# Kernel optimization log

Hardware: AMD Instinct MI355X
Metric: run time of the kernel (lower is better)

Reference implementation:

```python
import jax, jax.numpy as jnp
import numpy as np

D_MODEL = 1024
N_HEAD = 16
B, T = 4, 1024
MAX_REL = 32  # max_relative_positions


def setup_inputs() -> dict:
    key = jax.random.key(0)
    ks = jax.random.split(key, 12)
    s = 0.02
    inp = {
        "x": jax.random.normal(ks[0], (B, T, D_MODEL), jnp.float32),
        "mask": jnp.tril(jnp.ones((T, T), dtype=bool)),  # causal mask, 1 = keep
        "Wq": jax.random.normal(ks[1], (D_MODEL, D_MODEL), jnp.float32) * s,
        "bq": jax.random.normal(ks[2], (D_MODEL,), jnp.float32) * s,
        "Wk": jax.random.normal(ks[3], (D_MODEL, D_MODEL), jnp.float32) * s,
        "bk": jax.random.normal(ks[4], (D_MODEL,), jnp.float32) * s,
        "Wv": jax.random.normal(ks[5], (D_MODEL, D_MODEL), jnp.float32) * s,
        "bv": jax.random.normal(ks[6], (D_MODEL,), jnp.float32) * s,
        "Wo": jax.random.normal(ks[7], (D_MODEL, D_MODEL), jnp.float32) * s,
        "bo": jax.random.normal(ks[8], (D_MODEL,), jnp.float32) * s,
        "rel_bias": jax.random.normal(ks[9], (2 * MAX_REL - 1, N_HEAD), jnp.float32) * s,
        "n_head": N_HEAD,
    }
    return inp


def reference(x, mask, Wq, bq, Wk, bk, Wv, bv, Wo, bo, rel_bias, n_head):
    Bx, Tx, C = x.shape
    Dh = C // n_head
    scale = Dh ** (-0.5)
    # projections: torch Linear is x @ W.T + b
    Q = (x @ Wq.T + bq).reshape(Bx, Tx, n_head, Dh)
    K = (x @ Wk.T + bk).reshape(Bx, Tx, n_head, Dh)
    V = (x @ Wv.T + bv).reshape(Bx, Tx, n_head, Dh)
    # scores: [B, H, T, T]
    scores = jnp.einsum("bqhd,bkhd->bhqk", Q, K) * scale
    # T5-style clipped relative-position bias
    pos = jnp.arange(Tx)
    rel = pos[None, :] - pos[:, None]                     # k_pos - q_pos, [T, T]
    buckets = jnp.clip(rel, -(MAX_REL - 1), MAX_REL - 1) + (MAX_REL - 1)
    bias = rel_bias[buckets]                              # [T, T, H]
    scores = scores + jnp.transpose(bias, (2, 0, 1))[None]
    # original applies masked_fill(-inf) then masked_fill(0): net effect = 0
    scores = jnp.where(mask, scores, 0.0)
    w = jax.nn.relu(scores) + 1e-6
    w = jnp.where(mask, w, 0.0)
    w = w / (jnp.sum(w, axis=-1, keepdims=True) + 1e-6)
    out = jnp.einsum("bhqk,bkhd->bqhd", w, V).reshape(Bx, Tx, C)
    return out @ Wo.T + bo
```

## Files before the change

### kernel.cpp

```cpp
#include <hip/hip_runtime.h>


typedef __attribute__((ext_vector_type(8))) __bf16 bf16x8;
typedef __attribute__((ext_vector_type(4))) __bf16 bf16x4;
typedef __attribute__((ext_vector_type(4))) float f32x4;
typedef unsigned short u16;

__device__ __forceinline__ u16 f2bf(float f) {
  unsigned u = __float_as_uint(f);
  u += 0x7FFFu + ((u >> 16) & 1u);
  return (u16)(u >> 16);
}
__device__ __forceinline__ float bf2f(u16 b) {
  return __uint_as_float(((unsigned)b) << 16);
}
__device__ __forceinline__ void gl_lds16(const void* g, void* l) {
  __builtin_amdgcn_global_load_lds((__attribute__((address_space(1))) void*)g,
                                   (__attribute__((address_space(3))) void*)l,
                                   16, 0, 0);
}

__global__ __launch_bounds__(256) void cast_all_kernel(
    const float* __restrict__ x,  const float* __restrict__ wq,
    const float* __restrict__ wk, const float* __restrict__ wv,
    const float* __restrict__ wo,
    u16* __restrict__ xb, u16* __restrict__ wqb, u16* __restrict__ wkb,
    u16* __restrict__ wvb, u16* __restrict__ wob) {
  long i4 = (long)blockIdx.x * 256 + threadIdx.x;
  const float* src; u16* dst; long rel;
  if (i4 < 1048576) { src = x; dst = xb; rel = i4; }
  else {
    long j = i4 - 1048576;
    int w = (int)(j >> 18);
    rel = j & 262143;
    src = (w == 0) ? wq : (w == 1) ? wk : (w == 2) ? wv : wo;
    dst = (w == 0) ? wqb : (w == 1) ? wkb : (w == 2) ? wvb : wob;
  }
  float4 v = ((const float4*)src)[rel];
  ushort4 o;
  o.x = f2bf(v.x); o.y = f2bf(v.y); o.z = f2bf(v.z); o.w = f2bf(v.w);
  ((ushort4*)dst)[rel] = o;
}

template <bool STORE_BF16>
__device__ __forceinline__ void gemm_body(
    const u16* __restrict__ A, const u16* __restrict__ B,
    const float* __restrict__ bias, bool rowbias,
    void* __restrict__ Cout, int ldc, int m0, int n0) {
  constexpr int K = 1024;
  constexpr int NT = K / 64;
  __shared__ __align__(16) u16 As[2][128 * 64];
  __shared__ __align__(16) u16 Bs[2][128 * 64];

  const int t = threadIdx.x;
  const int lane = t & 63;
  const int wv = t >> 6;
  const int quad = lane >> 4;
  const int l15 = lane & 15;
  const int wr = wv >> 1, wc = wv & 1;
  const int sw0 = (quad ^ (l15 & 7)) * 8;
  const int sw1 = ((4 + quad) ^ (l15 & 7)) * 8;

  const f32x4 vzero = {0.f, 0.f, 0.f, 0.f};
  f32x4 acc[4][4];
#pragma unroll
  for (int i = 0; i < 4; ++i)
#pragma unroll
    for (int j = 0; j < 4; ++j) acc[i][j] = vzero;

  auto stage = [&](int kt, int bufi) {
#pragma unroll
    for (int p = 0; p < 4; ++p) {
      int idx = t + p * 256;
      int row = idx >> 3, seg = idx & 7;
      int sseg = seg ^ (row & 7);
      gl_lds16(&A[(long)(m0 + row) * K + kt * 64 + sseg * 8], &As[bufi][idx * 8]);
      gl_lds16(&B[(long)(n0 + row) * K + kt * 64 + sseg * 8], &Bs[bufi][idx * 8]);
    }
  };

  stage(0, 0);
  for (int kt = 0; kt < NT; ++kt) {
    const int bufi = kt & 1;
    if (kt + 1 < NT) {
      stage(kt + 1, bufi ^ 1);
      asm volatile("s_waitcnt vmcnt(8)" ::: "memory");
    } else {
      asm volatile("s_waitcnt vmcnt(0)" ::: "memory");
    }
    asm volatile("s_barrier" ::: "memory");
#pragma unroll
    for (int ks = 0; ks < 64; ks += 32) {
      const int sw = ks ? sw1 : sw0;
      bf16x8 af[4], bfg[4];
#pragma unroll
      for (int i = 0; i < 4; ++i)
        af[i] = *(const bf16x8*)&As[bufi][(wr * 64 + i * 16 + l15) * 64 + sw];
#pragma unroll
      for (int j = 0; j < 4; ++j)
        bfg[j] = *(const bf16x8*)&Bs[bufi][(wc * 64 + j * 16 + l15) * 64 + sw];
#pragma unroll
      for (int i = 0; i < 4; ++i)
#pragma unroll
        for (int j = 0; j < 4; ++j)
          acc[i][j] = __builtin_amdgcn_mfma_f32_16x16x32_bf16(af[i], bfg[j], acc[i][j], 0, 0, 0);
    }
    asm volatile("s_barrier" ::: "memory");
  }

  float cb[4];
  if (!rowbias) {
#pragma unroll
    for (int j = 0; j < 4; ++j) cb[j] = bias[n0 + wc * 64 + j * 16 + l15];
  }

#pragma unroll
  for (int i = 0; i < 4; ++i) {
#pragma unroll
    for (int r = 0; r < 4; ++r) {
      int row = m0 + wr * 64 + i * 16 + quad * 4 + r;
      long base = (long)row * ldc + n0 + wc * 64;
      float rb_ = rowbias ? bias[row] : 0.f;
#pragma unroll
      for (int j = 0; j < 4; ++j) {
        float v = acc[i][j][r] + (rowbias ? rb_ : cb[j]);
        if (STORE_BF16) ((u16*)Cout)[base + j * 16 + l15] = f2bf(v);
        else            ((float*)Cout)[base + j * 16 + l15] = v;
      }
    }
  }
}

__global__ __launch_bounds__(256) void gemm_qkv(
    const u16* __restrict__ xb, const u16* __restrict__ wqb,
    const u16* __restrict__ wkb, const u16* __restrict__ wvb,
    const float* __restrict__ bq, const float* __restrict__ bk,
    const float* __restrict__ bv,
    u16* __restrict__ Qb, u16* __restrict__ Kb, u16* __restrict__ Vtg) {
  const int bx = blockIdx.x;
  const u16 *AT, *BT;
  const float* bias;
  u16* C;
  int m0, n0, ldc;
  bool rowbias;
  if (bx < 512) {
    int g = bx >> 5;
    int sel = g >> 3;
    n0 = (g & 7) * 128; m0 = (bx & 31) * 128;
    AT = xb; BT = sel ? wkb : wqb; bias = sel ? bk : bq;
    C = sel ? Kb : Qb; ldc = 1024; rowbias = false;
  } else {
    int rem = bx - 512;
    n0 = (rem >> 3) * 128; m0 = (rem & 7) * 128;
    AT = wvb; BT = xb; bias = bv;
    C = Vtg; ldc = 4096; rowbias = true;
  }
  gemm_body<true>(AT, BT, bias, rowbias, C, ldc, m0, n0);
}

__global__ __launch_bounds__(256) void gemm_out(
    const u16* __restrict__ A, const u16* __restrict__ B,
    const float* __restrict__ bias, float* __restrict__ C) {
  gemm_body<false>(A, B, bias, false, C, 1024, blockIdx.x * 128, blockIdx.y * 128);
}

__global__ __launch_bounds__(512) void attn_strip(
    const u16* __restrict__ Qb,
    const u16* __restrict__ Kb,
    const u16* __restrict__ Vtg,
    const float* __restrict__ rel_bias,
    u16* __restrict__ att) {
  constexpr int WS = 68;
  __shared__ __align__(16) u16 Kt[64 * 64];
  __shared__ __align__(16) u16 Vt[64 * 64];
  __shared__ __align__(16) u16 Ws[8][16 * WS];
  __shared__ float biasl[64];

  const int bx = blockIdx.x;
  const int strip = 7 - (bx >> 6);
  const int bh = bx & 63;
  const int b = bh >> 4, h = bh & 15;
  const int q0 = strip * 128;
  const int cend = 2 * strip + 1;

  const int t = threadIdx.x;
  const int lane = t & 63;
  const int wv = t >> 6;
  const int quad = lane >> 4;
  const int l15 = lane & 15;

  if (t < 63) biasl[t] = rel_bias[t * 16 + h];
  const float b0c = rel_bias[h];

  const long qrow = (long)(b * 1024 + q0 + wv * 16 + l15) * 1024 + h * 64;
  bf16x8 qf0 = *(const bf16x8*)&Qb[qrow + quad * 8];
  bf16x8 qf1 = *(const bf16x8*)&Qb[qrow + 32 + quad * 8];

  const f32x4 vzero = {0.f, 0.f, 0.f, 0.f};
  f32x4 acc_o[4];
#pragma unroll
  for (int j = 0; j < 4; ++j) acc_o[j] = vzero;
  float denom = 0.f;
  const float scale = 0.125f;
  const int ql = q0 + wv * 16 + l15;
  const int sw0 = (quad ^ (l15 & 7)) * 8;
  const int sw1 = ((4 + quad) ^ (l15 & 7)) * 8;

  for (int c = 0; c <= cend; ++c) {
    const int k0 = c * 64;
    if (c) __syncthreads();
    {
      int row = t >> 3, seg = t & 7;
      int sw = row * 64 + ((seg ^ (row & 7)) * 8);
      uint4 kv = *(const uint4*)&Kb[(long)(b * 1024 + k0 + row) * 1024 + h * 64 + seg * 8];
      uint4 vvl = *(const uint4*)&Vtg[(long)(h * 64 + row) * 4096 + b * 1024 + k0 + seg * 8];
      *(uint4*)&Kt[sw] = kv;
      *(uint4*)&Vt[sw] = vvl;
    }
    __syncthreads();

    const bool fast = (c <= 2 * strip - 2);
#pragma unroll
    for (int g = 0; g < 4; ++g) {
      const u16* kr = &Kt[(g * 16 + l15) * 64];
      bf16x8 kf0 = *(const bf16x8*)&kr[sw0];
      bf16x8 kf1 = *(const bf16x8*)&kr[sw1];
      f32x4 sT = vzero;
      sT = __builtin_amdgcn_mfma_f32_16x16x32_bf16(kf0, qf0, sT, 0, 0, 0);
      sT = __builtin_amdgcn_mfma_f32_16x16x32_bf16(kf1, qf1, sT, 0, 0, 0);
      const int kgb = k0 + g * 16 + quad * 4;
      ushort4 wpk;
      if (fast) {
#pragma unroll
        for (int r = 0; r < 4; ++r) {
          float w = fmaxf(sT[r] * scale + b0c, 0.f) + 1e-6f;
          u16 wb = f2bf(w);
          denom += bf2f(wb);
          ((u16*)&wpk)[r] = wb;
        }
      } else {
#pragma unroll
        for (int r = 0; r < 4; ++r) {
          int kg = kgb + r;
          int dd = kg - ql;
          dd = dd < -31 ? -31 : (dd > 31 ? 31 : dd);
          float sv = sT[r] * scale + biasl[dd + 31];
          float w = (kg <= ql) ? (fmaxf(sv, 0.f) + 1e-6f) : 0.f;
          u16 wb = f2bf(w);
          denom += bf2f(wb);
          ((u16*)&wpk)[r] = wb;
        }
      }
      *(ushort4*)&Ws[wv][l15 * WS + g * 16 + quad * 4] = wpk;
    }
    asm volatile("s_waitcnt lgkmcnt(0)" ::: "memory");
#pragma unroll
    for (int ks = 0; ks < 64; ks += 32) {
      union { bf16x8 v8; bf16x4 v4[2]; } au;
      int wbase = l15 * WS + ks + quad * 8;
      au.v4[0] = *(const bf16x4*)&Ws[wv][wbase];
      au.v4[1] = *(const bf16x4*)&Ws[wv][wbase + 4];
      const int sv = ks ? sw1 : sw0;
#pragma unroll
      for (int j = 0; j < 4; ++j) {
        bf16x8 bvv = *(const bf16x8*)&Vt[(j * 16 + l15) * 64 + sv];
        acc_o[j] = __builtin_amdgcn_mfma_f32_16x16x32_bf16(au.v8, bvv, acc_o[j], 0, 0, 0);
      }
    }
  }

  denom += __shfl_xor(denom, 16);
  denom += __shfl_xor(denom, 32);

  float invm = 1.f / (denom + 1e-6f);
  float inv[4];
#pragma unroll
  for (int r = 0; r < 4; ++r) inv[r] = __shfl(invm, quad * 4 + r);
#pragma unroll
  for (int j = 0; j < 4; ++j)
#pragma unroll
    for (int r = 0; r < 4; ++r) {
      int q = q0 + wv * 16 + quad * 4 + r;
      att[(long)(b * 1024 + q) * 1024 + h * 64 + j * 16 + l15] = f2bf(acc_o[j][r] * inv[r]);
    }
}

extern "C" void kernel_launch(void* const* d_in, const int* in_sizes, int n_in,
                              void* d_out, int out_size, void* d_ws, size_t ws_size,
                              hipStream_t stream) {
  const float* x  = (const float*)d_in[0];
  const float* Wq = (const float*)d_in[2];
  const float* bq = (const float*)d_in[3];
  const float* Wk = (const float*)d_in[4];
  const float* bk = (const float*)d_in[5];
  const float* Wv = (const float*)d_in[6];
  const float* bv = (const float*)d_in[7];
  const float* Wo = (const float*)d_in[8];
  const float* bo = (const float*)d_in[9];
  const float* rb = (const float*)d_in[10];

  char* ws = (char*)d_ws;
  u16* xb  = (u16*)(ws);
  u16* wqb = (u16*)(ws + (8l  << 20));
  u16* wkb = (u16*)(ws + (10l << 20));
  u16* wvb = (u16*)(ws + (12l << 20));
  u16* wob = (u16*)(ws + (14l << 20));
  u16* Qb  = (u16*)(ws + (16l << 20));
  u16* Kb  = (u16*)d_out;
  u16* Vtg = (u16*)((char*)d_out + (8l << 20));

  cast_all_kernel<<<8192, 256, 0, stream>>>(x, Wq, Wk, Wv, Wo, xb, wqb, wkb, wvb, wob);
  gemm_qkv<<<768, 256, 0, stream>>>(xb, wqb, wkb, wvb, bq, bk, bv, Qb, Kb, Vtg);
  attn_strip<<<512, 512, 0, stream>>>(Qb, Kb, Vtg, rb, Qb);
  gemm_out<<<dim3(32, 8), 256, 0, stream>>>(Qb, wob, bo, (float*)d_out);
}
```

Measured before the change: 191.2 us.

## Use 256x256-tile 8-wave pipelined GEMM body for QKV projection

Replaces the 128x128 QKV GEMM with a 256x256-tile, 512-thread kernel. It uses double-buffered LDS split into two k-halves, async global-to-LDS loads interleaved with MFMA phases, setprio hints, and XOR-swizzled LDS layout. Blocks are remapped so consecutive block IDs spread across XCDs. The goal is more reuse per LDS load and better overlap of loads with compute. The cost is only 192 blocks on a 256-CU part, which may leave CUs idle, plus higher register and LDS pressure.

```diff
diff --git a/kernel.cpp b/kernel.cpp
--- a/kernel.cpp
+++ b/kernel.cpp
@@ -131,31 +131,177 @@
   }
 }
 
-__global__ __launch_bounds__(256) void gemm_qkv(
+template <bool STORE_BF16>
+__device__ __forceinline__ void gemm256_body(
+    const u16* __restrict__ A, const u16* __restrict__ B,
+    const float* __restrict__ bias, bool rowbias,
+    void* __restrict__ Cout, int ldc, int m0, int n0) {
+  constexpr int K = 1024;
+  constexpr int NT = K / 64;
+  __shared__ __align__(16) u16 As[2][2][256 * 32];
+  __shared__ __align__(16) u16 Bs[2][2][256 * 32];
+
+  const int t = threadIdx.x;
+  const int lane = t & 63;
+  const int wv = t >> 6;
+  const int wr = wv >> 2;
+  const int wc = wv & 3;
+  const int quad = lane >> 4;
+  const int l15 = lane & 15;
+
+  const int rA = wr * 128 + l15;
+  const int rB = wc * 64 + l15;
+  const int baseA = rA * 32 + ((quad ^ ((rA >> 1) & 3)) * 8);
+  const int baseB = rB * 32 + ((quad ^ ((rB >> 1) & 3)) * 8);
+
+  const int srow = t >> 2;
+  const int sg = (t & 3) ^ ((t >> 3) & 3);
+  const long sA = (long)(m0 + srow) * K + sg * 8;
+  const long sB = (long)(n0 + srow) * K + sg * 8;
+
+  auto stA = [&](int T_, int kh, int bf_) {
+    const u16* s = A + sA + T_ * 64 + kh * 32;
+    u16* d = &As[bf_][kh][t * 8];
+    gl_lds16(s, d);
+    gl_lds16(s + (long)128 * K, d + 4096);
+  };
+  auto stB = [&](int T_, int kh, int bf_) {
+    const u16* s = B + sB + T_ * 64 + kh * 32;
+    u16* d = &Bs[bf_][kh][t * 8];
+    gl_lds16(s, d);
+    gl_lds16(s + (long)128 * K, d + 4096);
+  };
+
+  const f32x4 vzero = {0.f, 0.f, 0.f, 0.f};
+  f32x4 acc[8][4];
+#pragma unroll
+  for (int i = 0; i < 8; ++i)
+#pragma unroll
+    for (int j = 0; j < 4; ++j) acc[i][j] = vzero;
+
+  stA(0, 0, 0); stB(0, 0, 0);
+  stA(0, 1, 0); stB(0, 1, 0);
+  stA(1, 0, 1); stB(1, 0, 1);
+  asm volatile("s_waitcnt vmcnt(4)" ::: "memory");
+  asm volatile("s_barrier" ::: "memory");
+
+  for (int T = 0; T < NT; ++T) {
+    const int c = T & 1;
+    const u16* Ac = &As[c][0][0];
+    const u16* Bc = &Bs[c][0][0];
+    bf16x8 af[4], bfr[4];
+
+#pragma unroll
+    for (int j = 0; j < 4; ++j) bfr[j] = *(const bf16x8*)&Bc[baseB + j * 512];
+#pragma unroll
+    for (int i = 0; i < 4; ++i) af[i] = *(const bf16x8*)&Ac[baseA + i * 512];
+    if (T + 1 < NT) stA(T + 1, 1, c ^ 1);
+    asm volatile("s_barrier" ::: "memory");
+    __builtin_amdgcn_s_setprio(1);
+#pragma unroll
+    for (int i = 0; i < 4; ++i)
+#pragma unroll
+      for (int j = 0; j < 4; ++j)
+        acc[i][j] = __builtin_amdgcn_mfma_f32_16x16x32_bf16(af[i], bfr[j], acc[i][j], 0, 0, 0);
+    __builtin_amdgcn_s_setprio(0);
+    asm volatile("s_barrier" ::: "memory");
+
+#pragma unroll
+    for (int i = 0; i < 4; ++i) af[i] = *(const bf16x8*)&Ac[baseA + 2048 + i * 512];
+    if (T + 1 < NT) stB(T + 1, 1, c ^ 1);
+    asm volatile("s_barrier" ::: "memory");
+    __builtin_amdgcn_s_setprio(1);
+#pragma unroll
+    for (int i = 0; i < 4; ++i)
+#pragma unroll
+      for (int j = 0; j < 4; ++j)
+        acc[4 + i][j] = __builtin_amdgcn_mfma_f32_16x16x32_bf16(af[i], bfr[j], acc[4 + i][j], 0, 0, 0);
+    __builtin_amdgcn_s_setprio(0);
+    asm volatile("s_barrier" ::: "memory");
+
+    if (T == NT - 1) {
+      asm volatile("s_waitcnt vmcnt(0)" ::: "memory");
+      asm volatile("s_barrier" ::: "memory");
+    }
+#pragma unroll
+    for (int j = 0; j < 4; ++j) bfr[j] = *(const bf16x8*)&Bc[8192 + baseB + j * 512];
+#pragma unroll
+    for (int i = 0; i < 4; ++i) af[i] = *(const bf16x8*)&Ac[8192 + baseA + i * 512];
+    if (T + 2 < NT) stA(T + 2, 0, c);
+    asm volatile("s_barrier" ::: "memory");
+    __builtin_amdgcn_s_setprio(1);
+#pragma unroll
+    for (int i = 0; i < 4; ++i)
+#pragma unroll
+      for (int j = 0; j < 4; ++j)
+        acc[i][j] = __builtin_amdgcn_mfma_f32_16x16x32_bf16(af[i], bfr[j], acc[i][j], 0, 0, 0);
+    __builtin_amdgcn_s_setprio(0);
+    asm volatile("s_barrier" ::: "memory");
+
+#pragma unroll
+    for (int i = 0; i < 4; ++i) af[i] = *(const bf16x8*)&Ac[8192 + baseA + 2048 + i * 512];
+    if (T + 2 < NT) stB(T + 2, 0, c);
+    asm volatile("s_barrier" ::: "memory");
+    __builtin_amdgcn_s_setprio(1);
+#pragma unroll
+    for (int i = 0; i < 4; ++i)
+#pragma unroll
+      for (int j = 0; j < 4; ++j)
+        acc[4 + i][j] = __builtin_amdgcn_mfma_f32_16x16x32_bf16(af[i], bfr[j], acc[4 + i][j], 0, 0, 0);
+    __builtin_amdgcn_s_setprio(0);
+    asm volatile("s_waitcnt vmcnt(4)" ::: "memory");
+    asm volatile("s_barrier" ::: "memory");
+  }
+
+  float cb[4];
+  if (!rowbias) {
+#pragma unroll
+    for (int j = 0; j < 4; ++j) cb[j] = bias[n0 + wc * 64 + j * 16 + l15];
+  }
+
+#pragma unroll
+  for (int mf = 0; mf < 8; ++mf) {
+#pragma unroll
+    for (int r = 0; r < 4; ++r) {
+      int row = m0 + wr * 128 + mf * 16 + quad * 4 + r;
+      long base = (long)row * ldc + n0 + wc * 64;
+      float rb_ = rowbias ? bias[row] : 0.f;
+#pragma unroll
+      for (int j = 0; j < 4; ++j) {
+        float v = acc[mf][j][r] + (rowbias ? rb_ : cb[j]);
+        if (STORE_BF16) ((u16*)Cout)[base + j * 16 + l15] = f2bf(v);
+        else            ((float*)Cout)[base + j * 16 + l15] = v;
+      }
+    }
+  }
+}
+
+__global__ __launch_bounds__(512, 2) void gemm_qkv(
     const u16* __restrict__ xb, const u16* __restrict__ wqb,
     const u16* __restrict__ wkb, const u16* __restrict__ wvb,
     const float* __restrict__ bq, const float* __restrict__ bk,
     const float* __restrict__ bv,
     u16* __restrict__ Qb, u16* __restrict__ Kb, u16* __restrict__ Vtg) {
   const int bx = blockIdx.x;
+  const int L = (bx & 7) * 24 + (bx >> 3);
   const u16 *AT, *BT;
   const float* bias;
   u16* C;
   int m0, n0, ldc;
   bool rowbias;
-  if (bx < 512) {
-    int g = bx >> 5;
-    int sel = g >> 3;
-    n0 = (g & 7) * 128; m0 = (bx & 31) * 128;
+  if (L < 128) {
+    int sel = L >> 6;
+    int g = L & 63;
+    m0 = (g >> 2) * 256; n0 = (g & 3) * 256;
     AT = xb; BT = sel ? wkb : wqb; bias = sel ? bk : bq;
     C = sel ? Kb : Qb; ldc = 1024; rowbias = false;
   } else {
-    int rem = bx - 512;
-    n0 = (rem >> 3) * 128; m0 = (rem & 7) * 128;
+    int g = L - 128;
+    m0 = (g & 3) * 256; n0 = (g >> 2) * 256;
     AT = wvb; BT = xb; bias = bv;
     C = Vtg; ldc = 4096; rowbias = true;
   }
-  gemm_body<true>(AT, BT, bias, rowbias, C, ldc, m0, n0);
+  gemm256_body<true>(AT, BT, bias, rowbias, C, ldc, m0, n0);
 }
 
 __global__ __launch_bounds__(256) void gemm_out(
@@ -310,7 +456,7 @@
   u16* Vtg = (u16*)((char*)d_out + (8l << 20));
 
   cast_all_kernel<<<8192, 256, 0, stream>>>(x, Wq, Wk, Wv, Wo, xb, wqb, wkb, wvb, wob);
-  gemm_qkv<<<768, 256, 0, stream>>>(xb, wqb, wkb, wvb, bq, bk, bv, Qb, Kb, Vtg);
+  gemm_qkv<<<192, 512, 0, stream>>>(xb, wqb, wkb, wvb, bq, bk, bv, Qb, Kb, Vtg);
   attn_strip<<<512, 512, 0, stream>>>(Qb, Kb, Vtg, rb, Qb);
   gemm_out<<<dim3(32, 8), 256, 0, stream>>>(Qb, wob, bo, (float*)d_out);
 }
```

Result: faster. 186.4 us (-2.5%).
